# Kernel optimization log

Measured on AMD Instinct MI355X. Metric: run time of the kernel, lower is better.

The kernel has to match this reference:

```python
import jax, jax.numpy as jnp
import numpy as np
from jax import lax


def setup_inputs() -> dict:
    key = jax.random.key(0)
    ks = jax.random.split(key, 6)
    B, C, H, W, K = 4, 4, 64, 64, 8192
    return {
        "x": jax.random.normal(ks[0], (B, C, H, W), dtype=jnp.float32),
        "prequant_w": jax.random.normal(ks[1], (C, C), dtype=jnp.float32) * 0.5,
        "prequant_b": jax.random.normal(ks[2], (C,), dtype=jnp.float32) * 0.1,
        "codebook": jax.random.normal(ks[3], (K, C), dtype=jnp.float32),
        "postquant_w": jax.random.normal(ks[4], (C, C), dtype=jnp.float32) * 0.5,
        "postquant_b": jax.random.normal(ks[5], (C,), dtype=jnp.float32) * 0.1,
    }


def reference(x, prequant_w, prequant_b, codebook, postquant_w, postquant_b):
    # x: [B, C, H, W] = encoder_out output (pre-prequant latent)
    B, C, H, W = x.shape
    N = H * W

    # prequant 1x1 conv
    q_in = jnp.einsum("bchw,oc->bohw", x, prequant_w) + prequant_b[None, :, None, None]
    feat_q = q_in.reshape(B, C, N).transpose(0, 2, 1)  # [B, N, C] (quant_in)
    feat_e = x.reshape(B, C, N).transpose(0, 2, 1)     # [B, N, C] ('out' in torch code)

    # cdist (p=2); argmin is invariant under sqrt so use squared distances
    # [B, N, K]
    sq_dist = (
        jnp.sum(feat_q * feat_q, axis=-1, keepdims=True)
        - 2.0 * jnp.einsum("bnc,kc->bnk", feat_q, codebook)
        + jnp.sum(codebook * codebook, axis=-1)
    )
    closest_idx = jnp.argmin(sq_dist, axis=-1)  # [B, N]

    quant = codebook[closest_idx]  # gather -> [B, N, C]

    codebook_loss = jnp.mean((quant - lax.stop_gradient(feat_e)) ** 2)
    commitment_loss = jnp.mean((lax.stop_gradient(quant) - feat_e) ** 2)

    # straight-through estimator
    st = feat_e + lax.stop_gradient(quant - feat_e)
    quant_map = st.transpose(0, 2, 1).reshape(B, C, H, W)

    # postquant 1x1 conv (first op of decode())
    dec_in = jnp.einsum("bchw,oc->bohw", quant_map, postquant_w) + postquant_b[None, :, None, None]

    return dec_in, codebook_loss, commitment_loss, closest_idx.reshape(B, H, W)
```

## Files before the change

kernel.cpp:

```cpp
#include <hip/hip_runtime.h>

#define BB 4
#define CC 4
#define NN 4096
#define KK 8192
#define NPOS 16384
#define SLICES 8
#define SLICE_K (KK / SLICES)
#define ITERS (SLICE_K / 64)
#define POSW 16

#define OUT_LOSS 65536
#define OUT_IDX  65538

#define KEYS_BYTES (NPOS * SLICES * 8)
#define QPRE_BYTE_OFF KEYS_BYTES
#define NRM_BYTE_OFF  (QPRE_BYTE_OFF + 8192 * 16 * 4)
#define ACC_BYTE_OFF  (NRM_BYTE_OFF + 8192 * 4)

typedef float v2f __attribute__((ext_vector_type(2)));

struct LossAcc { float sum; unsigned int cnt; };

__device__ __forceinline__ unsigned int fkey(float s) {
    unsigned int u = __float_as_uint(s);
    return (u & 0x80000000u) ? ~u : (u | 0x80000000u);
}

__device__ __forceinline__ unsigned long long shflx_u64(unsigned long long v, int m) {
    unsigned int lo = __shfl_xor((unsigned int)v, m, 64);
    unsigned int hi = __shfl_xor((unsigned int)(v >> 32), m, 64);
    return ((unsigned long long)hi << 32) | lo;
}

__global__ __launch_bounds__(256) void vq_pre(const float* __restrict__ x,
                                              const float* __restrict__ pw,
                                              const float* __restrict__ pb,
                                              const float* __restrict__ cb,
                                              float* __restrict__ qpre,
                                              float* __restrict__ nrm,
                                              LossAcc* __restrict__ acc) {
    int t = blockIdx.x * 256 + threadIdx.x;
    if (t == 0) { acc->sum = 0.0f; acc->cnt = 0u; }

    const float* e = cb + t * 4;
    float n0 = __fmul_rn(e[0], e[0]);
    n0 = __fadd_rn(n0, __fmul_rn(e[1], e[1]));
    n0 = __fadd_rn(n0, __fmul_rn(e[2], e[2]));
    n0 = __fadd_rn(n0, __fmul_rn(e[3], e[3]));
    nrm[t] = n0;

    int pos = 2 * t;
    int b = pos >> 12, n = pos & 4095;
    const float2* px = (const float2*)(x + b * (CC * NN) + n);
    float2 xv0 = px[0], xv1 = px[NN / 2], xv2 = px[NN], xv3 = px[3 * NN / 2];

    float qs[2][4], qqs[2];
#pragma unroll
    for (int h = 0; h < 2; ++h) {
        float a0 = h ? xv0.y : xv0.x, a1 = h ? xv1.y : xv1.x;
        float a2 = h ? xv2.y : xv2.x, a3 = h ? xv3.y : xv3.x;
#pragma unroll
        for (int o = 0; o < 4; ++o) {
            float tt = fmaf(pw[o * 4 + 0], a0, 0.0f);
            tt = fmaf(pw[o * 4 + 1], a1, tt);
            tt = fmaf(pw[o * 4 + 2], a2, tt);
            tt = fmaf(pw[o * 4 + 3], a3, tt);
            qs[h][o] = __fadd_rn(tt, pb[o]);
        }
        float s = __fmul_rn(qs[h][0], qs[h][0]);
        s = __fadd_rn(s, __fmul_rn(qs[h][1], qs[h][1]));
        s = __fadd_rn(s, __fmul_rn(qs[h][2], qs[h][2]));
        s = __fadd_rn(s, __fmul_rn(qs[h][3], qs[h][3]));
        qqs[h] = s;
    }

    float4* o4 = (float4*)(qpre + t * 16);
    o4[0] = make_float4(qs[0][0], qs[1][0], qs[0][1], qs[1][1]);
    o4[1] = make_float4(qs[0][2], qs[1][2], qs[0][3], qs[1][3]);
    ((float2*)(qpre + t * 16 + 8))[0] = make_float2(qqs[0], qqs[1]);
}

__global__ __launch_bounds__(64) void vq_search(const float* __restrict__ cb,
                                                const float* __restrict__ qpre,
                                                const float* __restrict__ nrm,
                                                unsigned long long* __restrict__ keys_ws) {
    __shared__ unsigned long long keys[POSW][64];

    const int lane  = threadIdx.x;
    const int gid   = blockIdx.x;
    const int slice = gid & (SLICES - 1);
    const int pg    = gid >> 3;
    const int k0    = slice * SLICE_K;

    v2f q2[8][4], qq2[8];
    const float* qp = qpre + (pg * 8) * 16;
#pragma unroll
    for (int g = 0; g < 8; ++g) {
        float4 a = ((const float4*)(qp + g * 16))[0];
        float4 b = ((const float4*)(qp + g * 16))[1];
        float2 c = ((const float2*)(qp + g * 16 + 8))[0];
        q2[g][0] = (v2f){a.x, a.y};
        q2[g][1] = (v2f){a.z, a.w};
        q2[g][2] = (v2f){b.x, b.y};
        q2[g][3] = (v2f){b.z, b.w};
        qq2[g]   = (v2f){c.x, c.y};
    }

    float best[POSW];
    int   bit_[POSW];
#pragma unroll
    for (int p = 0; p < POSW; ++p) { best[p] = __int_as_float(0x7f800000); bit_[p] = 0; }

    const float4* cb4 = (const float4*)cb + k0 + lane;
    const float*  nr  = nrm + k0 + lane;

#pragma unroll 4
    for (int it = 0; it < ITERS; ++it) {
        float4 e  = cb4[it * 64];
        float  nk = nr[it * 64];
        v2f nk2 = (v2f){nk, nk};
        v2f ex = (v2f){e.x, e.x}, ey = (v2f){e.y, e.y};
        v2f ez = (v2f){e.z, e.z}, ew = (v2f){e.w, e.w};
#pragma unroll
        for (int g = 0; g < 8; ++g) {
            v2f d = q2[g][0] * ex;
            d = __builtin_elementwise_fma(q2[g][1], ey, d);
            d = __builtin_elementwise_fma(q2[g][2], ez, d);
            d = __builtin_elementwise_fma(q2[g][3], ew, d);
            v2f s = __builtin_elementwise_fma((v2f){-2.0f, -2.0f}, d, qq2[g]);
            s = s + nk2;
            if (s.x < best[2 * g])     { best[2 * g]     = s.x; bit_[2 * g]     = it; }
            if (s.y < best[2 * g + 1]) { best[2 * g + 1] = s.y; bit_[2 * g + 1] = it; }
        }
    }

#pragma unroll
    for (int p = 0; p < POSW; ++p) {
        int kfull = k0 + lane + (bit_[p] << 6);
        keys[p][lane] = ((unsigned long long)fkey(best[p]) << 32) | (unsigned int)kfull;
    }
    __syncthreads();

    int p  = lane >> 2;
    int j0 = (lane & 3) << 4;
    unsigned long long bk = keys[p][j0];
#pragma unroll
    for (int j = 1; j < 16; ++j) {
        unsigned long long c = keys[p][j0 + j];
        bk = (c < bk) ? c : bk;
    }
#pragma unroll
    for (int m = 1; m < 4; m <<= 1) {
        unsigned long long c = shflx_u64(bk, m);
        bk = (c < bk) ? c : bk;
    }
    if ((lane & 3) == 0)
        keys_ws[(pg * POSW + p) * SLICES + slice] = bk;
}

__global__ __launch_bounds__(256) void vq_epi(const float* __restrict__ x,
                                              const float* __restrict__ cb,
                                              const float* __restrict__ qw,
                                              const float* __restrict__ qb,
                                              const unsigned long long* __restrict__ keys_ws,
                                              LossAcc* __restrict__ acc,
                                              float* __restrict__ out) {
    __shared__ float red[256];
    const int tid = threadIdx.x;
    const int pos = blockIdx.x * 256 + tid;

    unsigned long long bk = keys_ws[pos * SLICES + 0];
#pragma unroll
    for (int j = 1; j < SLICES; ++j) {
        unsigned long long c = keys_ws[pos * SLICES + j];
        bk = (c < bk) ? c : bk;
    }
    int idx = (int)(bk & 0xFFFFFFFFull);

    int b = pos >> 12, n = pos & 4095;
    const float4* cb4 = (const float4*)cb;
    float4 e = cb4[idx];

    const float* xb = x + b * (CC * NN) + n;
    float xv0 = xb[0], xv1 = xb[NN], xv2 = xb[2 * NN], xv3 = xb[3 * NN];

    float s0 = __fadd_rn(xv0, __fsub_rn(e.x, xv0));
    float s1 = __fadd_rn(xv1, __fsub_rn(e.y, xv1));
    float s2 = __fadd_rn(xv2, __fsub_rn(e.z, xv2));
    float s3 = __fadd_rn(xv3, __fsub_rn(e.w, xv3));

#pragma unroll
    for (int o = 0; o < 4; ++o) {
        float t = fmaf(qw[o * 4 + 0], s0, 0.0f);
        t = fmaf(qw[o * 4 + 1], s1, t);
        t = fmaf(qw[o * 4 + 2], s2, t);
        t = fmaf(qw[o * 4 + 3], s3, t);
        t = __fadd_rn(t, qb[o]);
        out[b * (CC * NN) + o * NN + n] = t;
    }

    out[OUT_IDX + b * NN + n] = (float)idx;

    float d0 = __fsub_rn(e.x, xv0), d1 = __fsub_rn(e.y, xv1);
    float d2 = __fsub_rn(e.z, xv2), d3 = __fsub_rn(e.w, xv3);
    float lp = __fmul_rn(d0, d0);
    lp = __fadd_rn(lp, __fmul_rn(d1, d1));
    lp = __fadd_rn(lp, __fmul_rn(d2, d2));
    lp = __fadd_rn(lp, __fmul_rn(d3, d3));

    red[tid] = lp;
    __syncthreads();
#pragma unroll
    for (int s = 128; s > 0; s >>= 1) {
        if (tid < s) red[tid] += red[tid + s];
        __syncthreads();
    }
    if (tid == 0) {
        atomicAdd(&acc->sum, red[0]);
        __threadfence();
        unsigned int old = atomicAdd(&acc->cnt, 1u);
        if (old == 63u) {
            float s = atomicAdd(&acc->sum, 0.0f);
            s *= (1.0f / (float)(NPOS * CC));
            out[OUT_LOSS + 0] = s;
            out[OUT_LOSS + 1] = s;
        }
    }
}

extern "C" void kernel_launch(void* const* d_in, const int* in_sizes, int n_in,
                              void* d_out, int out_size, void* d_ws, size_t ws_size,
                              hipStream_t stream) {
    const float* x  = (const float*)d_in[0];
    const float* pw = (const float*)d_in[1];
    const float* pb = (const float*)d_in[2];
    const float* cb = (const float*)d_in[3];
    const float* qw = (const float*)d_in[4];
    const float* qb = (const float*)d_in[5];
    float* out = (float*)d_out;

    unsigned long long* keys_ws = (unsigned long long*)d_ws;
    float* qpre  = (float*)((char*)d_ws + QPRE_BYTE_OFF);
    float* nrm   = (float*)((char*)d_ws + NRM_BYTE_OFF);
    LossAcc* acc = (LossAcc*)((char*)d_ws + ACC_BYTE_OFF);

    vq_pre<<<32, 256, 0, stream>>>(x, pw, pb, cb, qpre, nrm, acc);
    vq_search<<<(NPOS / POSW) * SLICES, 64, 0, stream>>>(cb, qpre, nrm, keys_ws);
    vq_epi<<<NPOS / 256, 256, 0, stream>>>(x, cb, qw, qb, keys_ws, acc, out);
}
```

Before: 98.01 us.

## Repartition codebook search into 256-thread blocks with fewer positions per wave

The search kernel now uses 256-thread blocks of four waves. Each wave handles 8 positions over a quarter of the codebook, instead of 64-thread blocks handling 16 positions over an eighth. This halves per-thread register state, which should raise occupancy, and halves the number of partial keys the epilogue must merge. In exchange each codebook load feeds half as many distance computations. The final in-block reduction becomes a serial 64-step scan done by 32 threads instead of the earlier shuffle-based reduction.

Result: slower. 100.5 us (+2.6%).

```diff
diff --git a/kernel.cpp b/kernel.cpp
--- a/kernel.cpp
+++ b/kernel.cpp
@@ -5,10 +5,10 @@
 #define NN 4096
 #define KK 8192
 #define NPOS 16384
-#define SLICES 8
+#define SLICES 4
 #define SLICE_K (KK / SLICES)
 #define ITERS (SLICE_K / 64)
-#define POSW 16
+#define POSW 8
 
 #define OUT_LOSS 65536
 #define OUT_IDX  65538
@@ -25,12 +25,6 @@
 __device__ __forceinline__ unsigned int fkey(float s) {
     unsigned int u = __float_as_uint(s);
     return (u & 0x80000000u) ? ~u : (u | 0x80000000u);
-}
-
-__device__ __forceinline__ unsigned long long shflx_u64(unsigned long long v, int m) {
-    unsigned int lo = __shfl_xor((unsigned int)v, m, 64);
-    unsigned int hi = __shfl_xor((unsigned int)(v >> 32), m, 64);
-    return ((unsigned long long)hi << 32) | lo;
 }
 
 __global__ __launch_bounds__(256) void vq_pre(const float* __restrict__ x,
@@ -81,22 +75,23 @@
     ((float2*)(qpre + t * 16 + 8))[0] = make_float2(qqs[0], qqs[1]);
 }
 
-__global__ __launch_bounds__(64) void vq_search(const float* __restrict__ cb,
-                                                const float* __restrict__ qpre,
-                                                const float* __restrict__ nrm,
-                                                unsigned long long* __restrict__ keys_ws) {
-    __shared__ unsigned long long keys[POSW][64];
-
-    const int lane  = threadIdx.x;
-    const int gid   = blockIdx.x;
-    const int slice = gid & (SLICES - 1);
-    const int pg    = gid >> 3;
+__global__ __launch_bounds__(256) void vq_search(const float* __restrict__ cb,
+                                                 const float* __restrict__ qpre,
+                                                 const float* __restrict__ nrm,
+                                                 unsigned long long* __restrict__ keys_ws) {
+    __shared__ unsigned long long keys[4][POSW][64];
+
+    const int tid   = threadIdx.x;
+    const int lane  = tid & 63;
+    const int wave  = tid >> 6;
+    const int slice = blockIdx.x & (SLICES - 1);
+    const int pg    = blockIdx.x >> 2;
     const int k0    = slice * SLICE_K;
 
-    v2f q2[8][4], qq2[8];
-    const float* qp = qpre + (pg * 8) * 16;
-#pragma unroll
-    for (int g = 0; g < 8; ++g) {
+    v2f q2[4][4], qq2[4];
+    const float* qp = qpre + ((pg * 4 + wave) * 4) * 16;
+#pragma unroll
+    for (int g = 0; g < 4; ++g) {
         float4 a = ((const float4*)(qp + g * 16))[0];
         float4 b = ((const float4*)(qp + g * 16))[1];
         float2 c = ((const float2*)(qp + g * 16 + 8))[0];
@@ -115,7 +110,7 @@
     const float4* cb4 = (const float4*)cb + k0 + lane;
     const float*  nr  = nrm + k0 + lane;
 
-#pragma unroll 4
+#pragma unroll 2
     for (int it = 0; it < ITERS; ++it) {
         float4 e  = cb4[it * 64];
         float  nk = nr[it * 64];
@@ -123,7 +118,7 @@
         v2f ex = (v2f){e.x, e.x}, ey = (v2f){e.y, e.y};
         v2f ez = (v2f){e.z, e.z}, ew = (v2f){e.w, e.w};
 #pragma unroll
-        for (int g = 0; g < 8; ++g) {
+        for (int g = 0; g < 4; ++g) {
             v2f d = q2[g][0] * ex;
             d = __builtin_elementwise_fma(q2[g][1], ey, d);
             d = __builtin_elementwise_fma(q2[g][2], ez, d);
@@ -138,25 +133,22 @@
 #pragma unroll
     for (int p = 0; p < POSW; ++p) {
         int kfull = k0 + lane + (bit_[p] << 6);
-        keys[p][lane] = ((unsigned long long)fkey(best[p]) << 32) | (unsigned int)kfull;
+        keys[wave][p][lane] =
+            ((unsigned long long)fkey(best[p]) << 32) | (unsigned int)kfull;
     }
     __syncthreads();
 
-    int p  = lane >> 2;
-    int j0 = (lane & 3) << 4;
-    unsigned long long bk = keys[p][j0];
-#pragma unroll
-    for (int j = 1; j < 16; ++j) {
-        unsigned long long c = keys[p][j0 + j];
-        bk = (c < bk) ? c : bk;
-    }
-#pragma unroll
-    for (int m = 1; m < 4; m <<= 1) {
-        unsigned long long c = shflx_u64(bk, m);
-        bk = (c < bk) ? c : bk;
-    }
-    if ((lane & 3) == 0)
-        keys_ws[(pg * POSW + p) * SLICES + slice] = bk;
+    if (tid < 32) {
+        int w = tid >> 3, p = tid & 7;
+        unsigned long long bk = ~0ull;
+#pragma unroll 4
+        for (int i = 0; i < 64; ++i) {
+            unsigned long long c = keys[w][p][i ^ tid];
+            bk = (c < bk) ? c : bk;
+        }
+        int pos = (pg * 4 + w) * 8 + p;
+        keys_ws[pos * SLICES + slice] = bk;
+    }
 }
 
 __global__ __launch_bounds__(256) void vq_epi(const float* __restrict__ x,
@@ -246,6 +238,6 @@
     LossAcc* acc = (LossAcc*)((char*)d_ws + ACC_BYTE_OFF);
 
     vq_pre<<<32, 256, 0, stream>>>(x, pw, pb, cb, qpre, nrm, acc);
-    vq_search<<<(NPOS / POSW) * SLICES, 64, 0, stream>>>(cb, qpre, nrm, keys_ws);
+    vq_search<<<(NPOS / 32) * SLICES, 256, 0, stream>>>(cb, qpre, nrm, keys_ws);
     vq_epi<<<NPOS / 256, 256, 0, stream>>>(x, cb, qw, qb, keys_ws, acc, out);
 }
```
